# Optimization experiments

Hardware: AMD Instinct MI355X
Metric: run time of the kernel (lower is better)

The kernel has to match this reference:

```python
import jax, jax.numpy as jnp
import numpy as np

BIG = 1e9  # self-distance masking constant, as in the torch module


def setup_inputs() -> dict:
    key = jax.random.key(0)
    k1, _ = jax.random.split(key)
    coords = jax.random.normal(k1, (8, 4096, 3), dtype=jnp.float32)
    mask = jnp.ones((8, 4096), dtype=bool)
    return {"coords": coords, "mask": mask}


def reference(coords, mask):
    # coords: [B, N, 3]; mask is accepted but unused (matches the torch module)
    B, N, _ = coords.shape
    # Pairwise Euclidean distances via the |a|^2 + |b|^2 - 2ab identity
    # (avoids materializing the [B,N,N,3] diff tensor the torch code builds).
    sq = jnp.sum(coords * coords, axis=-1)                      # [B, N]
    inner = jnp.einsum('bnd,bmd->bnm', coords, coords)          # [B, N, N]
    d2 = sq[:, :, None] + sq[:, None, :] - 2.0 * inner
    dist = jnp.sqrt(jnp.maximum(d2, 0.0))                       # [B, N, N]
    dist = dist + jnp.eye(N, dtype=dist.dtype) * BIG            # mask self
    # argsort(dim=2)[:, :, :2] == indices of the two smallest distances
    _, idx = jax.lax.top_k(-dist, 2)                            # [B, N, 2]
    first_nearest_indices = idx[:, :, 0]
    second_nearest_indices = idx[:, :, 1]
    A = jnp.take_along_axis(
        coords, jnp.broadcast_to(first_nearest_indices[:, :, None], (B, N, 3)), axis=1)
    C = jnp.take_along_axis(
        coords, jnp.broadcast_to(second_nearest_indices[:, :, None], (B, N, 3)), axis=1)
    return (A, C, first_nearest_indices, second_nearest_indices)
```

## Files before the change

kernel.cpp:

```cpp
#include <hip/hip_runtime.h>

#define BATCH 8
#define NPTS 4096
#define TOTQ (BATCH * NPTS)
#define TPB 256
#define NCH 64
#define CSZ 64
#define QF 8
#define BIGD 1e30f
#define MAXI 0x7fffffff

__device__ __forceinline__ float cand_w(float x, float y, float z) {
    return fmaf(x, x, fmaf(y, y, z * z));
}
__device__ __forceinline__ float cand_key(float cx, float cy, float cz, float w,
                                          float xn, float yn, float zn) {
    return fmaf(cx, xn, fmaf(cy, yn, fmaf(cz, zn, w)));
}

__device__ __forceinline__ void lexup(float k, int i,
                                      float& b1, int& i1,
                                      float& b2, int& i2) {
    bool c1 = (k < b1) || (k == b1 && i < i1);
    bool c2 = (k < b2) || (k == b2 && i < i2);
    float nb2 = c1 ? b1 : (c2 ? k : b2);
    int   ni2 = c1 ? i1 : (c2 ? i : i2);
    b1 = c1 ? k : b1;
    i1 = c1 ? i : i1;
    b2 = nb2;
    i2 = ni2;
}

__global__ __launch_bounds__(TPB) void knn_scan_v(const float* __restrict__ coords,
                                                  float2* __restrict__ vals) {
    __shared__ float4 pts[CSZ];
    const int tid   = (int)threadIdx.x;
    const int tile  = blockIdx.x;
    const int chunk = blockIdx.y;
    const int b     = blockIdx.z;
    const float* basep = coords + (size_t)b * NPTS * 3;
    const int mbase = chunk * CSZ;

    if (tid < CSZ) {
        float x = basep[(mbase + tid) * 3 + 0];
        float y = basep[(mbase + tid) * 3 + 1];
        float z = basep[(mbase + tid) * 3 + 2];
        pts[tid] = make_float4(-2.0f * x, -2.0f * y, -2.0f * z, cand_w(x, y, z));
    }

    const int qbase = tile * (TPB * QF);
    float xn[QF], yn[QF], zn[QF], b1[QF], b2[QF];
#pragma unroll
    for (int q = 0; q < QF; ++q) {
        int n = qbase + q * TPB + tid;
        xn[q] = basep[n * 3 + 0];
        yn[q] = basep[n * 3 + 1];
        zn[q] = basep[n * 3 + 2];
        b1[q] = BIGD; b2[q] = BIGD;
    }
    __syncthreads();

    for (int p = 0; p < CSZ; p += 4) {
        float4 c[4];
#pragma unroll
        for (int j = 0; j < 4; ++j) c[j] = pts[p + j];
#pragma unroll
        for (int j = 0; j < 4; ++j) {
#pragma unroll
            for (int q = 0; q < QF; ++q) {
                float k = cand_key(c[j].x, c[j].y, c[j].z, c[j].w, xn[q], yn[q], zn[q]);
                b2[q] = fminf(fmaxf(k, b1[q]), b2[q]);
                b1[q] = fminf(k, b1[q]);
            }
        }
    }

#pragma unroll
    for (int q = 0; q < QF; ++q) {
        int n = qbase + q * TPB + tid;
        vals[(size_t)chunk * TOTQ + (size_t)b * NPTS + n] = make_float2(b1[q], b2[q]);
    }
}

__global__ __launch_bounds__(TPB) void knn_merge_w(const float* __restrict__ coords,
                                                   const float2* __restrict__ vals,
                                                   float* __restrict__ out) {
    __shared__ float4 part[4][CSZ];
    __shared__ int4 rl[CSZ];
    __shared__ int2 res[CSZ];
    const int t  = (int)threadIdx.x;
    const int qi = t & 63;
    const int s  = t >> 6;
    const int qb = blockIdx.x * 64;
    const int q  = qb + qi;
    const int b  = qb >> 12;
    const int c_self = (qb & (NPTS - 1)) >> 6;
    const float* bp = coords + (size_t)b * NPTS * 3;

    float f1 = BIGD, f2 = BIGD;
    int t1 = MAXI, t2 = MAXI;
    for (int c = s * 16; c < s * 16 + 16; ++c) {
        if (c == c_self) continue;
        float2 v = vals[(size_t)c * TOTQ + q];
        lexup(v.x, 2 * c + 0, f1, t1, f2, t2);
        lexup(v.y, 2 * c + 1, f1, t1, f2, t2);
    }
    part[s][qi] = make_float4(f1, __int_as_float(t1), f2, __int_as_float(t2));
    __syncthreads();

    if (s == 0) {
#pragma unroll
        for (int ss = 1; ss < 4; ++ss) {
            float4 p = part[ss][qi];
            lexup(p.x, __float_as_int(p.y), f1, t1, f2, t2);
            lexup(p.z, __float_as_int(p.w), f1, t1, f2, t2);
        }
        const int ca = t1 >> 1;
        const int cb = t2 >> 1;
        const int lo = min(min(ca, cb), c_self);
        const int hi = max(max(ca, cb), c_self);
        const int md = ca + cb + c_self - lo - hi;
        rl[qi] = make_int4(lo, md, hi, 0);
    }
    __syncthreads();

    const int lane = qi;
    const int w = s;
    for (int j = 0; j < 16; ++j) {
        const int qj = w * 16 + j;
        const int4 r = rl[qj];
        const int n = (qb + qj) & (NPTS - 1);
        const float xq = bp[n * 3 + 0];
        const float yq = bp[n * 3 + 1];
        const float zq = bp[n * 3 + 2];

        float b1 = BIGD, b2 = BIGD;
        int i1 = MAXI, i2 = MAXI;
        int prev = -1;
#pragma unroll
        for (int u = 0; u < 3; ++u) {
            const int c = (u == 0) ? r.x : (u == 1) ? r.y : r.z;
            if (c == prev) continue;
            prev = c;
            const int m = c * CSZ + lane;
            const float x = bp[m * 3 + 0];
            const float y = bp[m * 3 + 1];
            const float z = bp[m * 3 + 2];
            const float wv = cand_w(x, y, z);
            float k = cand_key(-2.0f * x, -2.0f * y, -2.0f * z, wv, xq, yq, zq);
            const bool self = (m == n);
            k = self ? BIGD : k;
            lexup(k, self ? MAXI : m, b1, i1, b2, i2);
        }
#pragma unroll
        for (int off = 1; off < 64; off <<= 1) {
            const float ok1 = __shfl_xor(b1, off);
            const int   oi1 = __shfl_xor(i1, off);
            const float ok2 = __shfl_xor(b2, off);
            const int   oi2 = __shfl_xor(i2, off);
            lexup(ok1, oi1, b1, i1, b2, i2);
            lexup(ok2, oi2, b1, i1, b2, i2);
        }
        if (lane == 0) res[qj] = make_int2(i1, i2);
    }
    __syncthreads();

    if (s == 0) {
        const int i1 = res[qi].x;
        const int i2 = res[qi].y;
        float* A  = out;
        float* C  = out + (size_t)TOTQ * 3;
        float* I1 = out + (size_t)2 * TOTQ * 3;
        float* I2 = I1 + (size_t)TOTQ;
        A[(size_t)q * 3 + 0] = bp[i1 * 3 + 0];
        A[(size_t)q * 3 + 1] = bp[i1 * 3 + 1];
        A[(size_t)q * 3 + 2] = bp[i1 * 3 + 2];
        C[(size_t)q * 3 + 0] = bp[i2 * 3 + 0];
        C[(size_t)q * 3 + 1] = bp[i2 * 3 + 1];
        C[(size_t)q * 3 + 2] = bp[i2 * 3 + 2];
        I1[q] = (float)i1;
        I2[q] = (float)i2;
    }
}

__device__ __forceinline__ void top2min(float k, int m,
                                        float& b1, int& i1,
                                        float& b2, int& i2) {
    bool c1 = k < b1;
    bool c2 = k < b2;
    int ni2 = c2 ? m : i2;
    i2 = c1 ? i1 : ni2;
    i1 = c1 ? m : i1;
    b2 = fminf(fmaxf(k, b1), b2);
    b1 = fminf(k, b1);
}

__global__ __launch_bounds__(TPB) void knn_full(const float* __restrict__ coords,
                                                float* __restrict__ out) {
    __shared__ float4 pts[NPTS];
    const int tid  = (int)threadIdx.x;
    const int tile = blockIdx.x;
    const int b    = blockIdx.y;
    const float* basep = coords + (size_t)b * NPTS * 3;

    for (int p = tid; p < NPTS; p += TPB) {
        float x = basep[p * 3 + 0];
        float y = basep[p * 3 + 1];
        float z = basep[p * 3 + 2];
        pts[p] = make_float4(-2.0f * x, -2.0f * y, -2.0f * z, cand_w(x, y, z));
    }
    const int n = tile * TPB + tid;
    const float xn = basep[n * 3 + 0];
    const float yn = basep[n * 3 + 1];
    const float zn = basep[n * 3 + 2];
    __syncthreads();

    float b1 = BIGD, b2 = BIGD;
    int i1 = 0, i2 = 0;
    for (int p = 0; p < NPTS; p += 4) {
#pragma unroll
        for (int j = 0; j < 4; ++j) {
            float4 c = pts[p + j];
            float k = cand_key(c.x, c.y, c.z, c.w, xn, yn, zn);
            k = (p + j == n) ? BIGD : k;
            top2min(k, p + j, b1, i1, b2, i2);
        }
    }

    const int q = b * NPTS + n;
    float* A  = out;
    float* C  = out + (size_t)TOTQ * 3;
    float* I1 = out + (size_t)2 * TOTQ * 3;
    float* I2 = I1 + (size_t)TOTQ;
    float4 p1 = pts[i1];
    float4 p2 = pts[i2];
    A[(size_t)q * 3 + 0] = -0.5f * p1.x;
    A[(size_t)q * 3 + 1] = -0.5f * p1.y;
    A[(size_t)q * 3 + 2] = -0.5f * p1.z;
    C[(size_t)q * 3 + 0] = -0.5f * p2.x;
    C[(size_t)q * 3 + 1] = -0.5f * p2.y;
    C[(size_t)q * 3 + 2] = -0.5f * p2.z;
    I1[q] = (float)i1;
    I2[q] = (float)i2;
}

extern "C" void kernel_launch(void* const* d_in, const int* in_sizes, int n_in,
                              void* d_out, int out_size, void* d_ws, size_t ws_size,
                              hipStream_t stream) {
    const float* coords = (const float*)d_in[0];
    float* out = (float*)d_out;

    const size_t need = (size_t)NCH * TOTQ * sizeof(float2);
    if (ws_size >= need) {
        float2* vals = (float2*)d_ws;
        hipLaunchKernelGGL(knn_scan_v, dim3(NPTS / (TPB * QF), NCH, BATCH), dim3(TPB),
                           0, stream, coords, vals);
        hipLaunchKernelGGL(knn_merge_w, dim3(TOTQ / 64), dim3(TPB), 0, stream,
                           coords, vals, out);
    } else {
        hipLaunchKernelGGL(knn_full, dim3(NPTS / TPB, BATCH), dim3(TPB), 0, stream,
                           coords, out);
    }
}
```

Measured before the change: 123.9 us.

## Shrink merge kernel to 16 queries per block for more blocks and parallelism

The merge kernel now handles 16 queries per block instead of 64, launching four times as many blocks. Each thread scans 4 chunks rather than 16, and the final 16-way reduction runs in 16 threads. The refine stage loads all three candidate chunks' coordinates up front, with no dependent loop-carried skip. Output gather is spread across 48 threads. The aim is to shorten the serial per-thread work and raise occupancy and latency hiding in the merge pass, at the cost of more blocks, more barriers per query, and partly redundant loads.

```diff
diff --git a/kernel.cpp b/kernel.cpp
--- a/kernel.cpp
+++ b/kernel.cpp
@@ -7,6 +7,7 @@
 #define NCH 64
 #define CSZ 64
 #define QF 8
+#define QPB 16
 #define BIGD 1e30f
 #define MAXI 0x7fffffff
 
@@ -85,33 +86,39 @@
 __global__ __launch_bounds__(TPB) void knn_merge_w(const float* __restrict__ coords,
                                                    const float2* __restrict__ vals,
                                                    float* __restrict__ out) {
-    __shared__ float4 part[4][CSZ];
-    __shared__ int4 rl[CSZ];
-    __shared__ int2 res[CSZ];
+    __shared__ float4 part[16][QPB];
+    __shared__ int4 rl[QPB];
+    __shared__ int2 res[QPB];
     const int t  = (int)threadIdx.x;
-    const int qi = t & 63;
-    const int s  = t >> 6;
-    const int qb = blockIdx.x * 64;
-    const int q  = qb + qi;
+    const int qb = blockIdx.x * QPB;
     const int b  = qb >> 12;
     const int c_self = (qb & (NPTS - 1)) >> 6;
     const float* bp = coords + (size_t)b * NPTS * 3;
 
-    float f1 = BIGD, f2 = BIGD;
-    int t1 = MAXI, t2 = MAXI;
-    for (int c = s * 16; c < s * 16 + 16; ++c) {
-        if (c == c_self) continue;
-        float2 v = vals[(size_t)c * TOTQ + q];
-        lexup(v.x, 2 * c + 0, f1, t1, f2, t2);
-        lexup(v.y, 2 * c + 1, f1, t1, f2, t2);
-    }
-    part[s][qi] = make_float4(f1, __int_as_float(t1), f2, __int_as_float(t2));
-    __syncthreads();
-
-    if (s == 0) {
-#pragma unroll
-        for (int ss = 1; ss < 4; ++ss) {
-            float4 p = part[ss][qi];
+    {
+        const int s  = t >> 4;
+        const int qi = t & 15;
+        const int q  = qb + qi;
+        float f1 = BIGD, f2 = BIGD;
+        int t1 = MAXI, t2 = MAXI;
+#pragma unroll
+        for (int u = 0; u < 4; ++u) {
+            const int c = s * 4 + u;
+            if (c == c_self) continue;
+            float2 v = vals[(size_t)c * TOTQ + q];
+            lexup(v.x, 2 * c + 0, f1, t1, f2, t2);
+            lexup(v.y, 2 * c + 1, f1, t1, f2, t2);
+        }
+        part[s][qi] = make_float4(f1, __int_as_float(t1), f2, __int_as_float(t2));
+    }
+    __syncthreads();
+
+    if (t < QPB) {
+        float f1 = BIGD, f2 = BIGD;
+        int t1 = MAXI, t2 = MAXI;
+#pragma unroll
+        for (int ss = 0; ss < 16; ++ss) {
+            float4 p = part[ss][t];
             lexup(p.x, __float_as_int(p.y), f1, t1, f2, t2);
             lexup(p.z, __float_as_int(p.w), f1, t1, f2, t2);
         }
@@ -120,66 +127,79 @@
         const int lo = min(min(ca, cb), c_self);
         const int hi = max(max(ca, cb), c_self);
         const int md = ca + cb + c_self - lo - hi;
-        rl[qi] = make_int4(lo, md, hi, 0);
-    }
-    __syncthreads();
-
-    const int lane = qi;
-    const int w = s;
-    for (int j = 0; j < 16; ++j) {
-        const int qj = w * 16 + j;
-        const int4 r = rl[qj];
-        const int n = (qb + qj) & (NPTS - 1);
-        const float xq = bp[n * 3 + 0];
-        const float yq = bp[n * 3 + 1];
-        const float zq = bp[n * 3 + 2];
-
-        float b1 = BIGD, b2 = BIGD;
-        int i1 = MAXI, i2 = MAXI;
-        int prev = -1;
-#pragma unroll
-        for (int u = 0; u < 3; ++u) {
-            const int c = (u == 0) ? r.x : (u == 1) ? r.y : r.z;
-            if (c == prev) continue;
-            prev = c;
-            const int m = c * CSZ + lane;
-            const float x = bp[m * 3 + 0];
-            const float y = bp[m * 3 + 1];
-            const float z = bp[m * 3 + 2];
-            const float wv = cand_w(x, y, z);
-            float k = cand_key(-2.0f * x, -2.0f * y, -2.0f * z, wv, xq, yq, zq);
-            const bool self = (m == n);
-            k = self ? BIGD : k;
-            lexup(k, self ? MAXI : m, b1, i1, b2, i2);
-        }
-#pragma unroll
-        for (int off = 1; off < 64; off <<= 1) {
-            const float ok1 = __shfl_xor(b1, off);
-            const int   oi1 = __shfl_xor(i1, off);
-            const float ok2 = __shfl_xor(b2, off);
-            const int   oi2 = __shfl_xor(i2, off);
-            lexup(ok1, oi1, b1, i1, b2, i2);
-            lexup(ok2, oi2, b1, i1, b2, i2);
-        }
-        if (lane == 0) res[qj] = make_int2(i1, i2);
-    }
-    __syncthreads();
-
-    if (s == 0) {
-        const int i1 = res[qi].x;
-        const int i2 = res[qi].y;
-        float* A  = out;
-        float* C  = out + (size_t)TOTQ * 3;
+        rl[t] = make_int4(lo, md, hi, 0);
+    }
+    __syncthreads();
+
+    {
+        const int lane = t & 63;
+        const int w = t >> 6;
+        for (int j = 0; j < 4; ++j) {
+            const int qj = w * 4 + j;
+            const int4 r = rl[qj];
+            const int n = (qb + qj) & (NPTS - 1);
+            const float xq = bp[n * 3 + 0];
+            const float yq = bp[n * 3 + 1];
+            const float zq = bp[n * 3 + 2];
+
+            const int m0 = r.x * CSZ + lane;
+            const int m1 = r.y * CSZ + lane;
+            const int m2 = r.z * CSZ + lane;
+            float cx0 = bp[m0 * 3 + 0], cy0 = bp[m0 * 3 + 1], cz0 = bp[m0 * 3 + 2];
+            float cx1 = bp[m1 * 3 + 0], cy1 = bp[m1 * 3 + 1], cz1 = bp[m1 * 3 + 2];
+            float cx2 = bp[m2 * 3 + 0], cy2 = bp[m2 * 3 + 1], cz2 = bp[m2 * 3 + 2];
+
+            float b1 = BIGD, b2 = BIGD;
+            int i1 = MAXI, i2 = MAXI;
+            {
+                float k = cand_key(-2.0f * cx0, -2.0f * cy0, -2.0f * cz0,
+                                   cand_w(cx0, cy0, cz0), xq, yq, zq);
+                const bool self = (m0 == n);
+                lexup(self ? BIGD : k, self ? MAXI : m0, b1, i1, b2, i2);
+            }
+            if (r.y != r.x) {
+                float k = cand_key(-2.0f * cx1, -2.0f * cy1, -2.0f * cz1,
+                                   cand_w(cx1, cy1, cz1), xq, yq, zq);
+                const bool self = (m1 == n);
+                lexup(self ? BIGD : k, self ? MAXI : m1, b1, i1, b2, i2);
+            }
+            if (r.z != r.y) {
+                float k = cand_key(-2.0f * cx2, -2.0f * cy2, -2.0f * cz2,
+                                   cand_w(cx2, cy2, cz2), xq, yq, zq);
+                const bool self = (m2 == n);
+                lexup(self ? BIGD : k, self ? MAXI : m2, b1, i1, b2, i2);
+            }
+#pragma unroll
+            for (int off = 1; off < 64; off <<= 1) {
+                const float ok1 = __shfl_xor(b1, off);
+                const int   oi1 = __shfl_xor(i1, off);
+                const float ok2 = __shfl_xor(b2, off);
+                const int   oi2 = __shfl_xor(i2, off);
+                lexup(ok1, oi1, b1, i1, b2, i2);
+                lexup(ok2, oi2, b1, i1, b2, i2);
+            }
+            if (lane == 0) res[qj] = make_int2(i1, i2);
+        }
+    }
+    __syncthreads();
+
+    if (t < 48) {
+        const int qj = t / 3;
+        const int d  = t % 3;
+        const int q  = qb + qj;
+        const int i1 = res[qj].x;
+        const int i2 = res[qj].y;
+        float* A = out;
+        float* C = out + (size_t)TOTQ * 3;
+        A[(size_t)q * 3 + d] = bp[i1 * 3 + d];
+        C[(size_t)q * 3 + d] = bp[i2 * 3 + d];
+    }
+    if (t < QPB) {
+        const int q = qb + t;
         float* I1 = out + (size_t)2 * TOTQ * 3;
         float* I2 = I1 + (size_t)TOTQ;
-        A[(size_t)q * 3 + 0] = bp[i1 * 3 + 0];
-        A[(size_t)q * 3 + 1] = bp[i1 * 3 + 1];
-        A[(size_t)q * 3 + 2] = bp[i1 * 3 + 2];
-        C[(size_t)q * 3 + 0] = bp[i2 * 3 + 0];
-        C[(size_t)q * 3 + 1] = bp[i2 * 3 + 1];
-        C[(size_t)q * 3 + 2] = bp[i2 * 3 + 2];
-        I1[q] = (float)i1;
-        I2[q] = (float)i2;
+        I1[q] = (float)res[t].x;
+        I2[q] = (float)res[t].y;
     }
 }
 
@@ -255,7 +275,7 @@
         float2* vals = (float2*)d_ws;
         hipLaunchKernelGGL(knn_scan_v, dim3(NPTS / (TPB * QF), NCH, BATCH), dim3(TPB),
                            0, stream, coords, vals);
-        hipLaunchKernelGGL(knn_merge_w, dim3(TOTQ / 64), dim3(TPB), 0, stream,
+        hipLaunchKernelGGL(knn_merge_w, dim3(TOTQ / QPB), dim3(TPB), 0, stream,
                            coords, vals, out);
     } else {
         hipLaunchKernelGGL(knn_full, dim3(NPTS / TPB, BATCH), dim3(TPB), 0, stream,
```

Measured after the change: 99.76 us, median of 2. -19.5%, faster.
